# Kernel optimization log

Measured on AMD Instinct MI355X. Metric: run time of the kernel, lower is better.

Reference implementation:

```python
import jax, jax.numpy as jnp
import numpy as np
from functools import partial

NUM_HEADS = 2
HEAD_SIZE = 32


def rwkv6_block(x, Wr, Wk, Wv, Ww, Wo, u):
    """Canonical RWKV6 linear-attention block.
    x: [B,T,C]; W*: [C,C]; u: [H,K]. Returns (out [B,T,C], final_state [B,H,K,K]).
    """
    B, T, C = x.shape
    H, K = NUM_HEADS, HEAD_SIZE
    r = (x @ Wr).reshape(B, T, H, K)
    k = (x @ Wk).reshape(B, T, H, K)
    v = (x @ Wv).reshape(B, T, H, K)
    # data-dependent decay in (0,1)
    w = jnp.exp(-jnp.exp((x @ Ww).reshape(B, T, H, K)))

    def step(S, inp):
        r_t, k_t, v_t, w_t = inp  # each [B,H,K]
        kv = k_t[..., :, None] * v_t[..., None, :]          # [B,H,K,K] outer product
        o = jnp.einsum('bhk,bhkv->bhv', r_t, S + u[None, :, :, None] * kv)
        S = w_t[..., None] * S + kv                          # diag(w) decay
        return S, o

    # time-major for scan: [T,B,H,K]
    xs = (jnp.swapaxes(r, 0, 1), jnp.swapaxes(k, 0, 1),
          jnp.swapaxes(v, 0, 1), jnp.swapaxes(w, 0, 1))
    S0 = jnp.zeros((B, H, K, K), dtype=x.dtype)
    S_final, o = jax.lax.scan(step, S0, xs)                  # o: [T,B,H,K]
    o = jnp.swapaxes(o, 0, 1).reshape(B, T, C)
    return o @ Wo, S_final


def setup_inputs() -> dict:
    key = jax.random.key(0)
    ks = jax.random.split(key, 8)
    V, C, L = 32000, 64, 2
    B, T = 2, 4096
    s = 1.0 / np.sqrt(C)  # keep activations well-scaled
    return {
        'tokens': jax.random.randint(ks[0], (B, T), 0, V),
        'embed': jax.random.normal(ks[1], (V, C), jnp.float32) * s,
        'Wr': jax.random.normal(ks[2], (L, C, C), jnp.float32) * s,
        'Wk': jax.random.normal(ks[3], (L, C, C), jnp.float32) * s,
        'Wv': jax.random.normal(ks[4], (L, C, C), jnp.float32) * s,
        'Ww': jax.random.normal(ks[5], (L, C, C), jnp.float32) * s,
        'Wo': jax.random.normal(ks[6], (L, C, C), jnp.float32) * s,
        'u': jax.random.normal(ks[7], (L, NUM_HEADS, HEAD_SIZE), jnp.float32),
    }


def reference(tokens, embed, Wr, Wk, Wv, Ww, Wo, u):
    x = embed[tokens]                                        # [B,T,C] embedding lookup
    L = Wr.shape[0]
    for l in range(L):                                       # small fixed layer count
        out, _ = rwkv6_block(x, Wr[l], Wk[l], Wv[l], Ww[l], Wo[l], u[l])
        x = x + out                                          # residual
    return x @ embed.T                                       # tied-weight head -> logits [B,T,V]
```

## Files before the change

kernel.cpp:

```cpp
#include <hip/hip_runtime.h>

#define BB 2
#define TT 4096
#define CC 64
#define HH 2
#define KK 32
#define VV 32000
#define TC 64
#define NC (TT / TC)
#define NROWS (BB * TT)

__global__ __launch_bounds__(256) void k_embed(const int* __restrict__ tokens,
                                               const float* __restrict__ embed,
                                               float* __restrict__ X) {
  int id = blockIdx.x * 256 + threadIdx.x;
  int row = id >> 4, c4 = id & 15;
  int tok = tokens[row];
  ((float4*)X)[id] = ((const float4*)embed)[tok * 16 + c4];
}

__global__ __launch_bounds__(256) void k_proj(
    const float* __restrict__ X,
    const float* __restrict__ Wr, const float* __restrict__ Wk,
    const float* __restrict__ Wv, const float* __restrict__ Ww,
    float* __restrict__ Rb, float* __restrict__ Kb,
    float* __restrict__ Vb, float* __restrict__ Db) {
  int tid = threadIdx.x;
  int row0 = blockIdx.x * 16;
  int m = tid >> 6, j = tid & 63;
  const float* Wm = (m == 0) ? Wr : (m == 1) ? Wk : (m == 2) ? Wv : Ww;
  float* outp = (m == 0) ? Rb : (m == 1) ? Kb : (m == 2) ? Vb : Db;
  float wreg[64];
#pragma unroll
  for (int c = 0; c < 64; ++c) wreg[c] = Wm[c * 64 + j];
  for (int r = 0; r < 16; ++r) {
    float xv = X[(row0 + r) * 64 + j];
    float acc = 0.f;
#pragma unroll
    for (int c = 0; c < 64; ++c) acc = fmaf(__shfl(xv, c), wreg[c], acc);
    outp[(row0 + r) * 64 + j] = (m == 3) ? __expf(acc) : acc;
  }
}

__global__ __launch_bounds__(1024) void k_phase1(
    const float* __restrict__ Kb, const float* __restrict__ Vb,
    const float* __restrict__ Db, float* __restrict__ Ac,
    float* __restrict__ Bc) {
  __shared__ float kd[TC][KK];
  __shared__ float vt[TC][KK];
  __shared__ float dd[TC][KK];
  __shared__ float kk[TC][KK];
  int chunk = blockIdx.x, bh = blockIdx.y;
  int b = bh >> 1, h = bh & 1;
  int row0 = b * TT + chunk * TC;
  int cb = h * KK;
  int tid = threadIdx.x;
  for (int i = tid; i < TC * KK; i += 1024) {
    int t = i >> 5, k = i & 31;
    int g = (row0 + t) * CC + cb + k;
    dd[t][k] = Db[g];
    kk[t][k] = Kb[g];
    vt[t][k] = Vb[g];
  }
  __syncthreads();
  if (tid < KK) {
    int k = tid;
    float s = 0.f;
    for (int i = TC - 1; i >= 0; --i) {
      kd[i][k] = __expf(-s) * kk[i][k];
      s += dd[i][k];
    }
    Ac[(bh * NC + chunk) * KK + k] = __expf(-s);
  }
  __syncthreads();
  int k = tid >> 5, v = tid & 31;
  float acc = 0.f;
#pragma unroll 8
  for (int i = 0; i < TC; ++i) acc = fmaf(kd[i][k], vt[i][v], acc);
  Bc[((bh * NC + chunk) * KK + k) * KK + v] = acc;
}

__global__ __launch_bounds__(1024) void k_phase2(
    const float* __restrict__ Ac, const float* __restrict__ Bc,
    float* __restrict__ S0) {
  int bh = blockIdx.x;
  int tid = threadIdx.x;
  int k = tid >> 5, v = tid & 31;
  const float* Ab = Ac + bh * NC * KK;
  const float* Bb = Bc + bh * NC * KK * KK;
  float* Sb = S0 + bh * NC * KK * KK;
  float S = 0.f;
#pragma unroll 1
  for (int cc = 0; cc < NC; cc += 8) {
    float av[8], bv[8];
#pragma unroll
    for (int q = 0; q < 8; ++q) av[q] = Ab[(cc + q) * KK + k];
#pragma unroll
    for (int q = 0; q < 8; ++q) bv[q] = Bb[((cc + q) * KK + k) * KK + v];
#pragma unroll
    for (int q = 0; q < 8; ++q) {
      Sb[((cc + q) * KK + k) * KK + v] = S;
      S = fmaf(av[q], S, bv[q]);
    }
  }
}

__global__ __launch_bounds__(512) void k_phase3(
    const float* __restrict__ Rb, const float* __restrict__ Kb,
    const float* __restrict__ Vb, const float* __restrict__ Db,
    const float* __restrict__ S0, const float* __restrict__ u,
    float* __restrict__ O) {
  __shared__ float rs[TC][KK + 1];
  __shared__ float ks[TC][KK + 1];
  __shared__ float vs[TC][KK + 1];
  __shared__ float Ps[TC][KK + 1];
  __shared__ float Sc[TC][TC + 1];
  __shared__ float S0s[KK][KK + 1];
  __shared__ float us[KK];
  int chunk = blockIdx.x, bh = blockIdx.y;
  int b = bh >> 1, h = bh & 1;
  int row0 = b * TT + chunk * TC;
  int cb = h * KK;
  int tid = threadIdx.x;
  for (int i = tid; i < TC * KK; i += 512) {
    int t = i >> 5, k = i & 31;
    int g = (row0 + t) * CC + cb + k;
    rs[t][k] = Rb[g];
    ks[t][k] = Kb[g];
    vs[t][k] = Vb[g];
    Ps[t][k] = Db[g];
  }
  for (int i = tid; i < KK * KK; i += 512) {
    int k = i >> 5, v = i & 31;
    S0s[k][v] = S0[((bh * NC + chunk) * KK + k) * KK + v];
  }
  if (tid < KK) us[tid] = u[h * KK + tid];
  __syncthreads();
  if (tid < KK) {
    float run = 0.f;
    for (int t = 0; t < TC; ++t) {
      float dv = Ps[t][tid];
      Ps[t][tid] = run;
      run += dv;
    }
  }
  __syncthreads();
  for (int e = tid; e < TC * TC; e += 512) {
    int t = e >> 6, i = e & 63;
    float val = 0.f;
    if (i < t) {
#pragma unroll 8
      for (int k = 0; k < KK; ++k)
        val += rs[t][k] * ks[i][k] * __expf(Ps[i + 1][k] - Ps[t][k]);
    } else if (i == t) {
#pragma unroll 8
      for (int k = 0; k < KK; ++k) val += rs[t][k] * us[k] * ks[t][k];
    }
    Sc[t][i] = val;
  }
  __syncthreads();
  for (int i = tid; i < TC * KK; i += 512) {
    int t = i >> 5, k = i & 31;
    rs[t][k] *= __expf(-Ps[t][k]);
  }
  __syncthreads();
  for (int e = tid; e < TC * KK; e += 512) {
    int t = e >> 5, v = e & 31;
    float acc = 0.f;
    for (int i = 0; i <= t; ++i) acc = fmaf(Sc[t][i], vs[i][v], acc);
#pragma unroll 8
    for (int k = 0; k < KK; ++k) acc = fmaf(rs[t][k], S0s[k][v], acc);
    O[(row0 + t) * CC + cb + v] = acc;
  }
}

__global__ __launch_bounds__(256) void k_outproj(
    const float* __restrict__ O, const float* __restrict__ Wo,
    float* __restrict__ X) {
  int tid = threadIdx.x;
  int row0 = blockIdx.x * 16;
  int wv = tid >> 6, j = tid & 63;
  float wreg[64];
#pragma unroll
  for (int c = 0; c < 64; ++c) wreg[c] = Wo[c * 64 + j];
  for (int rr = 0; rr < 4; ++rr) {
    int row = row0 + wv * 4 + rr;
    float ov = O[row * 64 + j];
    float acc = 0.f;
#pragma unroll
    for (int c = 0; c < 64; ++c) acc = fmaf(__shfl(ov, c), wreg[c], acc);
    X[row * 64 + j] += acc;
  }
}

__global__ __launch_bounds__(256) void k_head(const float* __restrict__ X,
                                              const float* __restrict__ embed,
                                              float* __restrict__ out) {
  __shared__ __align__(16) float xs[128][64];
  __shared__ __align__(16) float es[64][128];
  int tid = threadIdx.x;
  int row0 = blockIdx.y * 128;
  int col0 = blockIdx.x * 128;
#pragma unroll
  for (int i = 0; i < 8; ++i) {
    int fi = i * 256 + tid;
    int r = fi >> 4, c4 = fi & 15;
    float4 t = *(const float4*)(X + (row0 + r) * 64 + c4 * 4);
    *(float4*)&xs[r][c4 * 4] = t;
  }
#pragma unroll
  for (int i = 0; i < 8; ++i) {
    int fi = i * 256 + tid;
    int v = fi >> 4, c4 = fi & 15;
    float4 t = *(const float4*)(embed + (col0 + v) * 64 + c4 * 4);
    es[c4 * 4 + 0][v] = t.x;
    es[c4 * 4 + 1][v] = t.y;
    es[c4 * 4 + 2][v] = t.z;
    es[c4 * 4 + 3][v] = t.w;
  }
  __syncthreads();
  int r0 = (tid >> 4) * 8, v0 = (tid & 15) * 8;
  float acc[8][8];
#pragma unroll
  for (int i = 0; i < 8; ++i)
#pragma unroll
    for (int j = 0; j < 8; ++j) acc[i][j] = 0.f;
  for (int cq = 0; cq < 64; cq += 4) {
    float4 xf[8];
#pragma unroll
    for (int i = 0; i < 8; ++i) xf[i] = *(const float4*)&xs[r0 + i][cq];
#pragma unroll
    for (int q = 0; q < 4; ++q) {
      float4 ea = *(const float4*)&es[cq + q][v0];
      float4 eb = *(const float4*)&es[cq + q][v0 + 4];
      float ev[8] = {ea.x, ea.y, ea.z, ea.w, eb.x, eb.y, eb.z, eb.w};
#pragma unroll
      for (int i = 0; i < 8; ++i) {
        float xv = (q == 0) ? xf[i].x : (q == 1) ? xf[i].y
                   : (q == 2) ? xf[i].z : xf[i].w;
#pragma unroll
        for (int j = 0; j < 8; ++j) acc[i][j] = fmaf(xv, ev[j], acc[i][j]);
      }
    }
  }
#pragma unroll
  for (int i = 0; i < 8; ++i) {
    float* op = out + (size_t)(row0 + r0 + i) * VV + col0 + v0;
    *(float4*)op = make_float4(acc[i][0], acc[i][1], acc[i][2], acc[i][3]);
    *(float4*)(op + 4) = make_float4(acc[i][4], acc[i][5], acc[i][6], acc[i][7]);
  }
}

extern "C" void kernel_launch(void* const* d_in, const int* in_sizes, int n_in,
                              void* d_out, int out_size, void* d_ws,
                              size_t ws_size, hipStream_t stream) {
  const int* tokens = (const int*)d_in[0];
  const float* embed = (const float*)d_in[1];
  const float* Wr = (const float*)d_in[2];
  const float* Wk = (const float*)d_in[3];
  const float* Wv = (const float*)d_in[4];
  const float* Ww = (const float*)d_in[5];
  const float* Wo = (const float*)d_in[6];
  const float* u = (const float*)d_in[7];
  float* out = (float*)d_out;

  float* X = (float*)d_ws;
  float* Rb = X + NROWS * CC;
  float* Kb = Rb + NROWS * CC;
  float* Vb = Kb + NROWS * CC;
  float* Db = Vb + NROWS * CC;
  float* O = Db + NROWS * CC;
  float* Ac = O + NROWS * CC;
  float* Bc = Ac + BB * HH * NC * KK;
  float* S0 = Bc + BB * HH * NC * KK * KK;

  k_embed<<<NROWS * 16 / 256, 256, 0, stream>>>(tokens, embed, X);
  for (int l = 0; l < 2; ++l) {
    const float* Wrl = Wr + l * CC * CC;
    const float* Wkl = Wk + l * CC * CC;
    const float* Wvl = Wv + l * CC * CC;
    const float* Wwl = Ww + l * CC * CC;
    const float* Wol = Wo + l * CC * CC;
    const float* ul = u + l * HH * KK;
    k_proj<<<NROWS / 16, 256, 0, stream>>>(X, Wrl, Wkl, Wvl, Wwl, Rb, Kb, Vb,
                                           Db);
    k_phase1<<<dim3(NC, BB * HH), 1024, 0, stream>>>(Kb, Vb, Db, Ac, Bc);
    k_phase2<<<BB * HH, 1024, 0, stream>>>(Ac, Bc, S0);
    k_phase3<<<dim3(NC, BB * HH), 512, 0, stream>>>(Rb, Kb, Vb, Db, S0, ul, O);
    k_outproj<<<NROWS / 16, 256, 0, stream>>>(O, Wol, X);
  }
  k_head<<<dim3(VV / 128, NROWS / 128), 256, 0, stream>>>(X, embed, out);
}
```

Measured before the change: 1.442 ms.

## Compute tied-embedding head with split-bf16 MFMA (3-term hi/lo emulation)

Replaces the FP32 SIMT logits GEMM with a matrix-core kernel. X and the embedding are each split into bf16 high and low parts, and the product is rebuilt as hi*hi + hi*lo + lo*hi using the 16x16x32 bf16 MFMA. This is meant to cut the compute cost of the large [8192x64]x[64x32000] head while keeping close to FP32 accuracy. It adds two split kernels and extra workspace, loads fragments straight from global memory with no LDS, and writes scalar stores that are only partly coalesced.

```diff
diff --git a/kernel.cpp b/kernel.cpp
--- a/kernel.cpp
+++ b/kernel.cpp
@@ -9,6 +9,9 @@
 #define TC 64
 #define NC (TT / TC)
 #define NROWS (BB * TT)
+
+typedef __attribute__((ext_vector_type(8))) short short8;
+typedef __attribute__((ext_vector_type(4))) float f32x4;
 
 __global__ __launch_bounds__(256) void k_embed(const int* __restrict__ tokens,
                                                const float* __restrict__ embed,
@@ -193,62 +196,85 @@
   }
 }
 
-__global__ __launch_bounds__(256) void k_head(const float* __restrict__ X,
-                                              const float* __restrict__ embed,
-                                              float* __restrict__ out) {
-  __shared__ __align__(16) float xs[128][64];
-  __shared__ __align__(16) float es[64][128];
-  int tid = threadIdx.x;
-  int row0 = blockIdx.y * 128;
-  int col0 = blockIdx.x * 128;
-#pragma unroll
-  for (int i = 0; i < 8; ++i) {
-    int fi = i * 256 + tid;
-    int r = fi >> 4, c4 = fi & 15;
-    float4 t = *(const float4*)(X + (row0 + r) * 64 + c4 * 4);
-    *(float4*)&xs[r][c4 * 4] = t;
-  }
-#pragma unroll
-  for (int i = 0; i < 8; ++i) {
-    int fi = i * 256 + tid;
-    int v = fi >> 4, c4 = fi & 15;
-    float4 t = *(const float4*)(embed + (col0 + v) * 64 + c4 * 4);
-    es[c4 * 4 + 0][v] = t.x;
-    es[c4 * 4 + 1][v] = t.y;
-    es[c4 * 4 + 2][v] = t.z;
-    es[c4 * 4 + 3][v] = t.w;
-  }
-  __syncthreads();
-  int r0 = (tid >> 4) * 8, v0 = (tid & 15) * 8;
-  float acc[8][8];
-#pragma unroll
-  for (int i = 0; i < 8; ++i)
-#pragma unroll
-    for (int j = 0; j < 8; ++j) acc[i][j] = 0.f;
-  for (int cq = 0; cq < 64; cq += 4) {
-    float4 xf[8];
-#pragma unroll
-    for (int i = 0; i < 8; ++i) xf[i] = *(const float4*)&xs[r0 + i][cq];
-#pragma unroll
-    for (int q = 0; q < 4; ++q) {
-      float4 ea = *(const float4*)&es[cq + q][v0];
-      float4 eb = *(const float4*)&es[cq + q][v0 + 4];
-      float ev[8] = {ea.x, ea.y, ea.z, ea.w, eb.x, eb.y, eb.z, eb.w};
-#pragma unroll
-      for (int i = 0; i < 8; ++i) {
-        float xv = (q == 0) ? xf[i].x : (q == 1) ? xf[i].y
-                   : (q == 2) ? xf[i].z : xf[i].w;
-#pragma unroll
-        for (int j = 0; j < 8; ++j) acc[i][j] = fmaf(xv, ev[j], acc[i][j]);
-      }
-    }
-  }
-#pragma unroll
-  for (int i = 0; i < 8; ++i) {
-    float* op = out + (size_t)(row0 + r0 + i) * VV + col0 + v0;
-    *(float4*)op = make_float4(acc[i][0], acc[i][1], acc[i][2], acc[i][3]);
-    *(float4*)(op + 4) = make_float4(acc[i][4], acc[i][5], acc[i][6], acc[i][7]);
-  }
+__global__ __launch_bounds__(256) void k_split(const float* __restrict__ src,
+                                               unsigned short* __restrict__ hi,
+                                               unsigned short* __restrict__ lo,
+                                               int n4) {
+  int id = blockIdx.x * 256 + threadIdx.x;
+  if (id >= n4) return;
+  float4 x = ((const float4*)src)[id];
+  float xs[4] = {x.x, x.y, x.z, x.w};
+  unsigned short h[4], l[4];
+#pragma unroll
+  for (int i = 0; i < 4; ++i) {
+    unsigned int b = __float_as_uint(xs[i]);
+    unsigned int hb = b & 0xFFFF0000u;
+    h[i] = (unsigned short)(hb >> 16);
+    float lof = xs[i] - __uint_as_float(hb);
+    unsigned int lb = __float_as_uint(lof);
+    lb += 0x7FFFu + ((lb >> 16) & 1u);
+    l[i] = (unsigned short)(lb >> 16);
+  }
+  ((ushort4*)hi)[id] = make_ushort4(h[0], h[1], h[2], h[3]);
+  ((ushort4*)lo)[id] = make_ushort4(l[0], l[1], l[2], l[3]);
+}
+
+__global__ __launch_bounds__(256) void k_head_mfma(
+    const unsigned short* __restrict__ Xhi, const unsigned short* __restrict__ Xlo,
+    const unsigned short* __restrict__ Ehi, const unsigned short* __restrict__ Elo,
+    float* __restrict__ out) {
+  int tid = threadIdx.x;
+  int wave = tid >> 6, lane = tid & 63;
+  int lg = lane >> 4, lr = lane & 15;
+  int row0 = blockIdx.y * 64 + (wave & 1) * 32;
+  int col0 = blockIdx.x * 128 + (wave >> 1) * 64;
+
+  f32x4 acc[2][4];
+#pragma unroll
+  for (int rt = 0; rt < 2; ++rt)
+#pragma unroll
+    for (int ct = 0; ct < 4; ++ct) acc[rt][ct] = (f32x4){0.f, 0.f, 0.f, 0.f};
+
+  const unsigned short* Asrc[3] = {Xhi, Xhi, Xlo};
+  const unsigned short* Bsrc[3] = {Ehi, Elo, Ehi};
+
+#pragma unroll
+  for (int term = 0; term < 3; ++term) {
+    const unsigned short* A = Asrc[term];
+    const unsigned short* B = Bsrc[term];
+    short8 a[2][2], bfr[2][4];
+#pragma unroll
+    for (int rt = 0; rt < 2; ++rt)
+#pragma unroll
+      for (int kk2 = 0; kk2 < 2; ++kk2)
+        a[rt][kk2] = *(const short8*)(A + (size_t)(row0 + rt * 16 + lr) * CC +
+                                      kk2 * 32 + lg * 8);
+#pragma unroll
+    for (int ct = 0; ct < 4; ++ct)
+#pragma unroll
+      for (int kk2 = 0; kk2 < 2; ++kk2)
+        bfr[kk2][ct] = *(const short8*)(B + (size_t)(col0 + ct * 16 + lr) * CC +
+                                        kk2 * 32 + lg * 8);
+#pragma unroll
+    for (int rt = 0; rt < 2; ++rt)
+#pragma unroll
+      for (int ct = 0; ct < 4; ++ct)
+#pragma unroll
+        for (int kk2 = 0; kk2 < 2; ++kk2)
+          acc[rt][ct] = __builtin_amdgcn_mfma_f32_16x16x32_bf16(
+              a[rt][kk2], bfr[kk2][ct], acc[rt][ct], 0, 0, 0);
+  }
+
+#pragma unroll
+  for (int rt = 0; rt < 2; ++rt)
+#pragma unroll
+    for (int ct = 0; ct < 4; ++ct) {
+      int col = col0 + ct * 16 + lr;
+      int rbase = row0 + rt * 16 + lg * 4;
+#pragma unroll
+      for (int rg = 0; rg < 4; ++rg)
+        out[(size_t)(rbase + rg) * VV + col] = acc[rt][ct][rg];
+    }
 }
 
 extern "C" void kernel_launch(void* const* d_in, const int* in_sizes, int n_in,
@@ -273,8 +299,14 @@
   float* Ac = O + NROWS * CC;
   float* Bc = Ac + BB * HH * NC * KK;
   float* S0 = Bc + BB * HH * NC * KK * KK;
+  unsigned short* Ehi = (unsigned short*)(S0 + BB * HH * NC * KK * KK);
+  unsigned short* Elo = Ehi + (size_t)VV * CC;
+  unsigned short* Xhi = Elo + (size_t)VV * CC;
+  unsigned short* Xlo = Xhi + (size_t)NROWS * CC;
 
   k_embed<<<NROWS * 16 / 256, 256, 0, stream>>>(tokens, embed, X);
+  k_split<<<(VV * CC / 4 + 255) / 256, 256, 0, stream>>>(embed, Ehi, Elo,
+                                                         VV * CC / 4);
   for (int l = 0; l < 2; ++l) {
     const float* Wrl = Wr + l * CC * CC;
     const float* Wkl = Wk + l * CC * CC;
@@ -289,5 +321,8 @@
     k_phase3<<<dim3(NC, BB * HH), 512, 0, stream>>>(Rb, Kb, Vb, Db, S0, ul, O);
     k_outproj<<<NROWS / 16, 256, 0, stream>>>(O, Wol, X);
   }
-  k_head<<<dim3(VV / 128, NROWS / 128), 256, 0, stream>>>(X, embed, out);
-}
+  k_split<<<(NROWS * CC / 4 + 255) / 256, 256, 0, stream>>>(X, Xhi, Xlo,
+                                                            NROWS * CC / 4);
+  k_head_mfma<<<dim3(VV / 128, NROWS / 64), 256, 0, stream>>>(Xhi, Xlo, Ehi,
+                                                              Elo, out);
+}
```

Result: faster. 1.403 ms (-2.7%).
